# Performance work log

Hardware: AMD Instinct MI355X
Metric: run time of the kernel (lower is better)

The kernel has to match this reference:

```python
import jax, jax.numpy as jnp
import numpy as np

TOP_K = 2


def setup_inputs() -> dict:
    key = jax.random.key(0)
    k1, k2 = jax.random.split(key)
    x = jax.random.normal(k1, (4, 4096, 2048), dtype=jnp.float32)
    W = jax.random.normal(k2, (64, 2048), dtype=jnp.float32) * (1.0 / np.sqrt(2048))
    return {"x": x, "W": W}


def reference(x, W):
    B, S, D = x.shape
    E = W.shape[0]
    # logits: [B*S, E] via linear router (no bias)
    flat = x.reshape(-1, D)
    logits = jnp.einsum('td,ed->te', flat, W)
    probs = jax.nn.softmax(logits, axis=-1)
    # eval path: top-k indices
    _, top_k_indices = jax.lax.top_k(probs, TOP_K)          # [T, K]
    # scatter 1s -> mask; scatter gathered probs -> router_probs (== probs*mask)
    router_mask = jax.nn.one_hot(top_k_indices, E, dtype=probs.dtype).sum(axis=-2)  # [T, E]
    router_probs = probs * router_mask
    # normalize (top_k > 1: gradient flows through the sum)
    router_probs = router_probs / router_probs.sum(axis=-1, keepdims=True)
    return (router_mask.reshape(B, S, E),
            top_k_indices.reshape(B, S, TOP_K),
            router_probs.reshape(B, S, E),
            probs.reshape(B, S, E))
```

## Files before the change

kernel.cpp:

```cpp
#include <hip/hip_runtime.h>
#include <math.h>


#define D_DIM 2048
#define E_DIM 64
#define TPB 16
#define KSPLIT 4
#define KSTEPS 16

typedef __bf16 bf16x8 __attribute__((ext_vector_type(8)));
typedef unsigned short us8 __attribute__((ext_vector_type(8)));
typedef float f32x4 __attribute__((ext_vector_type(4)));

static __device__ __forceinline__ unsigned short f2bf(float f) {
    unsigned int u = __float_as_uint(f);
    u += 0x7fffu + ((u >> 16) & 1u);
    return (unsigned short)(u >> 16);
}
static __device__ __forceinline__ float bf2f(unsigned short h) {
    return __uint_as_float(((unsigned int)h) << 16);
}
static __device__ __forceinline__ void split4(const float4 v, ushort4* h, ushort4* l) {
    h->x = f2bf(v.x); l->x = f2bf(v.x - bf2f(h->x));
    h->y = f2bf(v.y); l->y = f2bf(v.y - bf2f(h->y));
    h->z = f2bf(v.z); l->z = f2bf(v.z - bf2f(h->z));
    h->w = f2bf(v.w); l->w = f2bf(v.w - bf2f(h->w));
}

__global__ __launch_bounds__(256, 1) void convert_w(
    const float4* __restrict__ W4, unsigned short* __restrict__ WH,
    unsigned short* __restrict__ WL)
{
    int i = blockIdx.x * 256 + threadIdx.x;
    float4 v = W4[i];
    ushort4 h, l;
    split4(v, &h, &l);
    *(ushort4*)&WH[i * 4] = h;
    *(ushort4*)&WL[i * 4] = l;
}

__global__ __launch_bounds__(256, 4) void router_fused(
    const float* __restrict__ x,
    const unsigned short* __restrict__ WH, const unsigned short* __restrict__ WL,
    float* __restrict__ mask_out, float* __restrict__ idx_out,
    float* __restrict__ rp_out, float* __restrict__ probs_out)
{
    __shared__ float PART[KSPLIT * 64 * 16];
    __shared__ float LG[TPB * 65];

    const int tid  = threadIdx.x;
    const int lane = tid & 63;
    const int wv   = tid >> 6;
    const int quad = lane >> 4;
    const int l16  = lane & 15;
    const int t0   = blockIdx.x * TPB;

    const float4* x4 = (const float4*)x;
    const size_t xbase = (size_t)(t0 + l16) * 512 + wv * 128 + quad * 2;
    const int wbase = l16 * 2048 + wv * 512 + quad * 8;

    f32x4 acc[4];
    #pragma unroll
    for (int n = 0; n < 4; ++n) { f32x4 z = {0.f, 0.f, 0.f, 0.f}; acc[n] = z; }

    float4 xa = x4[xbase];
    float4 xb = x4[xbase + 1];

    for (int ks = 0; ks < KSTEPS; ++ks) {
        ushort4 h0, l0, h1, l1;
        split4(xa, &h0, &l0);
        split4(xb, &h1, &l1);
        union { us8 u; bf16x8 b; } ua, ul;
        ua.u = (us8){h0.x, h0.y, h0.z, h0.w, h1.x, h1.y, h1.z, h1.w};
        ul.u = (us8){l0.x, l0.y, l0.z, l0.w, l1.x, l1.y, l1.z, l1.w};
        bf16x8 ah = ua.b, al = ul.b;

        if (ks + 1 < KSTEPS) {
            xa = x4[xbase + (ks + 1) * 8];
            xb = x4[xbase + (ks + 1) * 8 + 1];
        }

        const int ko = ks * 32;
        #pragma unroll
        for (int n = 0; n < 4; ++n) {
            bf16x8 bh = *(const bf16x8*)(WH + wbase + n * 32768 + ko);
            bf16x8 bl = *(const bf16x8*)(WL + wbase + n * 32768 + ko);
            acc[n] = __builtin_amdgcn_mfma_f32_16x16x32_bf16(ah, bh, acc[n], 0, 0, 0);
            acc[n] = __builtin_amdgcn_mfma_f32_16x16x32_bf16(al, bh, acc[n], 0, 0, 0);
            acc[n] = __builtin_amdgcn_mfma_f32_16x16x32_bf16(ah, bl, acc[n], 0, 0, 0);
        }
    }

    #pragma unroll
    for (int n = 0; n < 4; ++n)
        #pragma unroll
        for (int r = 0; r < 4; ++r)
            PART[wv * 1024 + lane * 16 + n * 4 + r] = acc[n][r];
    __syncthreads();

    #pragma unroll
    for (int c = 0; c < 4; ++c) {
        int idx = tid * 4 + c;
        int t = idx >> 6, e = idx & 63;
        int off = ((t >> 2) * 16 + (e & 15)) * 16 + ((e >> 4) * 4 + (t & 3));
        LG[t * 65 + e] = PART[off] + PART[1024 + off] + PART[2048 + off] + PART[3072 + off];
    }
    __syncthreads();

    for (int i = 0; i < 4; ++i) {
        int tl = wv * 4 + i;
        float v = LG[tl * 65 + lane];

        float bv = v; int bi = lane;
        #pragma unroll
        for (int off = 1; off < 64; off <<= 1) {
            float ov = __shfl_xor(bv, off, 64);
            int   oi = __shfl_xor(bi, off, 64);
            bool take = (ov > bv) || (ov == bv && oi < bi);
            bv = take ? ov : bv;
            bi = take ? oi : bi;
        }
        float m = bv; int i1 = bi;

        float p = __expf(v - m);
        float s = p;
        #pragma unroll
        for (int off = 1; off < 64; off <<= 1) s += __shfl_xor(s, off, 64);
        float prob = p / s;

        float v2 = (lane == i1) ? -INFINITY : v;
        float bv2 = v2; int bi2 = lane;
        #pragma unroll
        for (int off = 1; off < 64; off <<= 1) {
            float ov = __shfl_xor(bv2, off, 64);
            int   oi = __shfl_xor(bi2, off, 64);
            bool take = (ov > bv2) || (ov == bv2 && oi < bi2);
            bv2 = take ? ov : bv2;
            bi2 = take ? oi : bi2;
        }
        int i2 = bi2;

        float pd = __shfl(prob, i1, 64) + __shfl(prob, i2, 64);
        int t = t0 + tl;
        bool top = (lane == i1) || (lane == i2);

        mask_out[t * 64 + lane]  = top ? 1.f : 0.f;
        rp_out[t * 64 + lane]    = top ? prob / pd : 0.f;
        probs_out[t * 64 + lane] = prob;
        if (lane == 0) {
            idx_out[t * 2]     = (float)i1;
            idx_out[t * 2 + 1] = (float)i2;
        }
    }
}

extern "C" void kernel_launch(void* const* d_in, const int* in_sizes, int n_in,
                              void* d_out, int out_size, void* d_ws, size_t ws_size,
                              hipStream_t stream) {
    const float* x = (const float*)d_in[0];
    const float* W = (const float*)d_in[1];
    float* out = (float*)d_out;

    const int T = in_sizes[0] / D_DIM;
    const int WN = in_sizes[1];

    unsigned short* WH = (unsigned short*)d_ws;
    unsigned short* WL = WH + WN;

    float* mask_out  = out;
    float* idx_out   = out + (size_t)T * E_DIM;
    float* rp_out    = idx_out + (size_t)T * 2;
    float* probs_out = rp_out + (size_t)T * E_DIM;

    convert_w<<<dim3(WN / 4 / 256), dim3(256), 0, stream>>>((const float4*)W, WH, WL);
    router_fused<<<dim3(T / TPB), dim3(256), 0, stream>>>(
        x, WH, WL, mask_out, idx_out, rp_out, probs_out);
}
```

Before: 253.3 us.

## Split router into LDS-tiled split-K GEMM plus separate reduce/top-k kernel

Replaces the single fused kernel, which used 16-token blocks reading W straight from global memory, with a GEMM kernel that handles 64-token tiles. It stages x and the bf16 hi/lo W chunks into swizzled LDS through global_load_lds, and splits the K dimension across blocks that write partial logits to the workspace. A second kernel sums the partials and does softmax, top-2 and the output writes. The aim is more W reuse per block and better load efficiency. The cost is an extra partial-logit round trip through global memory, one more launch, and a barrier per chunk with no double buffering.

```diff
diff --git a/kernel.cpp b/kernel.cpp
--- a/kernel.cpp
+++ b/kernel.cpp
@@ -4,9 +4,6 @@
 
 #define D_DIM 2048
 #define E_DIM 64
-#define TPB 16
-#define KSPLIT 4
-#define KSTEPS 16
 
 typedef __bf16 bf16x8 __attribute__((ext_vector_type(8)));
 typedef unsigned short us8 __attribute__((ext_vector_type(8)));
@@ -25,6 +22,13 @@
     h->y = f2bf(v.y); l->y = f2bf(v.y - bf2f(h->y));
     h->z = f2bf(v.z); l->z = f2bf(v.z - bf2f(h->z));
     h->w = f2bf(v.w); l->w = f2bf(v.w - bf2f(h->w));
+}
+
+static __device__ __forceinline__ void gld_lds16(const void* g, void* l) {
+    __builtin_amdgcn_global_load_lds(
+        (const __attribute__((address_space(1))) unsigned int*)g,
+        (__attribute__((address_space(3))) unsigned int*)l,
+        16, 0, 0);
 }
 
 __global__ __launch_bounds__(256, 1) void convert_w(
@@ -39,77 +43,111 @@
     *(ushort4*)&WL[i * 4] = l;
 }
 
-__global__ __launch_bounds__(256, 4) void router_fused(
+template<int KS>
+__global__ __launch_bounds__(256, 4) void gemm_part(
     const float* __restrict__ x,
-    const unsigned short* __restrict__ WH, const unsigned short* __restrict__ WL,
-    float* __restrict__ mask_out, float* __restrict__ idx_out,
-    float* __restrict__ rp_out, float* __restrict__ probs_out)
+    const unsigned short* __restrict__ WHg, const unsigned short* __restrict__ WLg,
+    float* __restrict__ P, int T)
 {
-    __shared__ float PART[KSPLIT * 64 * 16];
-    __shared__ float LG[TPB * 65];
+    __shared__ __align__(16) float          XF [64 * 64];
+    __shared__ __align__(16) unsigned short WHs[64 * 64];
+    __shared__ __align__(16) unsigned short WLs[64 * 64];
 
     const int tid  = threadIdx.x;
     const int lane = tid & 63;
     const int wv   = tid >> 6;
     const int quad = lane >> 4;
     const int l16  = lane & 15;
-    const int t0   = blockIdx.x * TPB;
-
-    const float4* x4 = (const float4*)x;
-    const size_t xbase = (size_t)(t0 + l16) * 512 + wv * 128 + quad * 2;
-    const int wbase = l16 * 2048 + wv * 512 + quad * 8;
+
+    const int ntb = T >> 6;
+    const int tb  = blockIdx.x % ntb;
+    const int ksl = blockIdx.x / ntb;
+    const int t0  = tb << 6;
+    const int NCH = (D_DIM / KS) >> 6;
+    const int k0  = ksl * (D_DIM / KS);
 
     f32x4 acc[4];
     #pragma unroll
     for (int n = 0; n < 4; ++n) { f32x4 z = {0.f, 0.f, 0.f, 0.f}; acc[n] = z; }
 
-    float4 xa = x4[xbase];
-    float4 xb = x4[xbase + 1];
-
-    for (int ks = 0; ks < KSTEPS; ++ks) {
-        ushort4 h0, l0, h1, l1;
-        split4(xa, &h0, &l0);
-        split4(xb, &h1, &l1);
-        union { us8 u; bf16x8 b; } ua, ul;
-        ua.u = (us8){h0.x, h0.y, h0.z, h0.w, h1.x, h1.y, h1.z, h1.w};
-        ul.u = (us8){l0.x, l0.y, l0.z, l0.w, l1.x, l1.y, l1.z, l1.w};
-        bf16x8 ah = ua.b, al = ul.b;
-
-        if (ks + 1 < KSTEPS) {
-            xa = x4[xbase + (ks + 1) * 8];
-            xb = x4[xbase + (ks + 1) * 8 + 1];
-        }
-
-        const int ko = ks * 32;
-        #pragma unroll
-        for (int n = 0; n < 4; ++n) {
-            bf16x8 bh = *(const bf16x8*)(WH + wbase + n * 32768 + ko);
-            bf16x8 bl = *(const bf16x8*)(WL + wbase + n * 32768 + ko);
-            acc[n] = __builtin_amdgcn_mfma_f32_16x16x32_bf16(ah, bh, acc[n], 0, 0, 0);
-            acc[n] = __builtin_amdgcn_mfma_f32_16x16x32_bf16(al, bh, acc[n], 0, 0, 0);
-            acc[n] = __builtin_amdgcn_mfma_f32_16x16x32_bf16(ah, bl, acc[n], 0, 0, 0);
-        }
+    const int srow = wv * 4 + (lane >> 4);
+    const int scg  = lane & 15;
+    const int we   = wv * 8 + (lane >> 3);
+    const int wo   = lane & 7;
+
+    for (int ch = 0; ch < NCH; ++ch) {
+        const int kc = k0 + (ch << 6);
+
+        #pragma unroll
+        for (int i = 0; i < 4; ++i) {
+            int row = i * 16 + srow;
+            int cg  = scg ^ (row & 15);
+            gld_lds16(x + (size_t)(t0 + row) * D_DIM + kc + cg * 4,
+                      &XF[(i * 256 + wv * 64) * 4]);
+        }
+        #pragma unroll
+        for (int i2 = 0; i2 < 2; ++i2) {
+            int e  = i2 * 32 + we;
+            int og = wo ^ (e & 7);
+            gld_lds16(WHg + (size_t)e * D_DIM + kc + og * 8,
+                      &WHs[(i2 * 256 + wv * 64) * 8]);
+            gld_lds16(WLg + (size_t)e * D_DIM + kc + og * 8,
+                      &WLs[(i2 * 256 + wv * 64) * 8]);
+        }
+        __syncthreads();
+
+        #pragma unroll
+        for (int ks = 0; ks < 2; ++ks) {
+            const int tr = wv * 16 + l16;
+            const int c0 = ks * 8 + quad * 2;
+            float4 xa = *(const float4*)&XF[(tr * 16 + ( c0      ^ (tr & 15))) * 4];
+            float4 xb = *(const float4*)&XF[(tr * 16 + ((c0 + 1) ^ (tr & 15))) * 4];
+            ushort4 h0, l0, h1, l1;
+            split4(xa, &h0, &l0);
+            split4(xb, &h1, &l1);
+            union { us8 u; bf16x8 b; } ua, ul;
+            ua.u = (us8){h0.x, h0.y, h0.z, h0.w, h1.x, h1.y, h1.z, h1.w};
+            ul.u = (us8){l0.x, l0.y, l0.z, l0.w, l1.x, l1.y, l1.z, l1.w};
+
+            #pragma unroll
+            for (int n = 0; n < 4; ++n) {
+                int e = n * 16 + l16;
+                int o = ks * 4 + quad;
+                int s = e * 8 + (o ^ (e & 7));
+                bf16x8 bh = *(const bf16x8*)&WHs[s * 8];
+                bf16x8 bl = *(const bf16x8*)&WLs[s * 8];
+                acc[n] = __builtin_amdgcn_mfma_f32_16x16x32_bf16(ua.b, bh, acc[n], 0, 0, 0);
+                acc[n] = __builtin_amdgcn_mfma_f32_16x16x32_bf16(ul.b, bh, acc[n], 0, 0, 0);
+                acc[n] = __builtin_amdgcn_mfma_f32_16x16x32_bf16(ua.b, bl, acc[n], 0, 0, 0);
+            }
+        }
+        __syncthreads();
     }
 
+    float* Pb = P + ((size_t)ksl * T + t0) * 64;
     #pragma unroll
     for (int n = 0; n < 4; ++n)
         #pragma unroll
         for (int r = 0; r < 4; ++r)
-            PART[wv * 1024 + lane * 16 + n * 4 + r] = acc[n][r];
-    __syncthreads();
-
-    #pragma unroll
-    for (int c = 0; c < 4; ++c) {
-        int idx = tid * 4 + c;
-        int t = idx >> 6, e = idx & 63;
-        int off = ((t >> 2) * 16 + (e & 15)) * 16 + ((e >> 4) * 4 + (t & 3));
-        LG[t * 65 + e] = PART[off] + PART[1024 + off] + PART[2048 + off] + PART[3072 + off];
-    }
-    __syncthreads();
+            Pb[(wv * 16 + quad * 4 + r) * 64 + n * 16 + l16] = acc[n][r];
+}
+
+template<int KS>
+__global__ __launch_bounds__(256, 4) void reduce_router(
+    const float* __restrict__ P, int T,
+    float* __restrict__ mask_out, float* __restrict__ idx_out,
+    float* __restrict__ rp_out, float* __restrict__ probs_out)
+{
+    const int tid  = threadIdx.x;
+    const int lane = tid & 63;
+    const int wv   = tid >> 6;
 
     for (int i = 0; i < 4; ++i) {
-        int tl = wv * 4 + i;
-        float v = LG[tl * 65 + lane];
+        int t = blockIdx.x * 16 + wv * 4 + i;
+        float v = 0.f;
+        #pragma unroll
+        for (int s = 0; s < KS; ++s)
+            v += P[((size_t)s * T + t) * 64 + lane];
 
         float bv = v; int bi = lane;
         #pragma unroll
@@ -141,15 +179,14 @@
         int i2 = bi2;
 
         float pd = __shfl(prob, i1, 64) + __shfl(prob, i2, 64);
-        int t = t0 + tl;
         bool top = (lane == i1) || (lane == i2);
 
-        mask_out[t * 64 + lane]  = top ? 1.f : 0.f;
-        rp_out[t * 64 + lane]    = top ? prob / pd : 0.f;
-        probs_out[t * 64 + lane] = prob;
+        mask_out[(size_t)t * 64 + lane]  = top ? 1.f : 0.f;
+        rp_out[(size_t)t * 64 + lane]    = top ? prob / pd : 0.f;
+        probs_out[(size_t)t * 64 + lane] = prob;
         if (lane == 0) {
-            idx_out[t * 2]     = (float)i1;
-            idx_out[t * 2 + 1] = (float)i2;
+            idx_out[(size_t)t * 2]     = (float)i1;
+            idx_out[(size_t)t * 2 + 1] = (float)i2;
         }
     }
 }
@@ -161,18 +198,34 @@
     const float* W = (const float*)d_in[1];
     float* out = (float*)d_out;
 
-    const int T = in_sizes[0] / D_DIM;
+    const int T  = in_sizes[0] / D_DIM;
     const int WN = in_sizes[1];
 
     unsigned short* WH = (unsigned short*)d_ws;
     unsigned short* WL = WH + WN;
+    float* P = (float*)(WL + WN);
 
     float* mask_out  = out;
     float* idx_out   = out + (size_t)T * E_DIM;
     float* rp_out    = idx_out + (size_t)T * 2;
     float* probs_out = rp_out + (size_t)T * E_DIM;
 
-    convert_w<<<dim3(WN / 4 / 256), dim3(256), 0, stream>>>((const float4*)W, WH, WL);
-    router_fused<<<dim3(T / TPB), dim3(256), 0, stream>>>(
-        x, WH, WL, mask_out, idx_out, rp_out, probs_out);
-}
+    const size_t avail = ws_size - (size_t)WN * 4;
+    const size_t slice_bytes = (size_t)T * 64 * 4;
+
+    convert_w<<<dim3(WN / 1024), dim3(256), 0, stream>>>((const float4*)W, WH, WL);
+
+    if (avail >= 4 * slice_bytes) {
+        gemm_part<4><<<dim3((T / 64) * 4), dim3(256), 0, stream>>>(x, WH, WL, P, T);
+        reduce_router<4><<<dim3(T / 16), dim3(256), 0, stream>>>(
+            P, T, mask_out, idx_out, rp_out, probs_out);
+    } else if (avail >= 2 * slice_bytes) {
+        gemm_part<2><<<dim3((T / 64) * 2), dim3(256), 0, stream>>>(x, WH, WL, P, T);
+        reduce_router<2><<<dim3(T / 16), dim3(256), 0, stream>>>(
+            P, T, mask_out, idx_out, rp_out, probs_out);
+    } else {
+        gemm_part<1><<<dim3(T / 64), dim3(256), 0, stream>>>(x, WH, WL, P, T);
+        reduce_router<1><<<dim3(T / 16), dim3(256), 0, stream>>>(
+            P, T, mask_out, idx_out, rp_out, probs_out);
+    }
+}
```

Result: faster. 208.3 us (-17.8%).
